# Kernel optimization log

Measured on AMD Instinct MI355X. Metric: run time of the kernel, lower is better.

## Reference

```python
import jax, jax.numpy as jnp
import numpy as np

HEADS = (4, 2, 1)
OUTS = (32, 16, 2)
NEG_SLOPE = 0.2


def gat_conv(x, src, dst, W, att_s, att_d, b, heads, out_dim, n_nodes, concat):
    # x: [N, Fin] -> h: [N, H, Fout]
    h = (x @ W).reshape(n_nodes, heads, out_dim)
    # per-node attention terms, gathered to edges: [E, H]
    a_src = jnp.sum(h * att_s, axis=-1)
    a_dst = jnp.sum(h * att_d, axis=-1)
    logits = jax.nn.leaky_relu(a_src[src] + a_dst[dst], NEG_SLOPE)
    # segment softmax over incoming edges of each destination node
    lmax = jax.ops.segment_max(logits, dst, num_segments=n_nodes)[dst]
    e = jnp.exp(logits - lmax)
    denom = jax.ops.segment_sum(e, dst, num_segments=n_nodes)[dst]
    alpha = e / denom  # [E, H]
    # weighted message aggregation
    msg = h[src] * alpha[:, :, None]  # [E, H, Fout]
    agg = jax.ops.segment_sum(msg, dst, num_segments=n_nodes)  # [N, H, Fout]
    if concat:
        agg = agg.reshape(n_nodes, heads * out_dim)
    else:
        agg = agg.mean(axis=1)
    return agg + b


def _glorot(key, shape):
    fan = shape[0] + shape[-1] if len(shape) == 2 else shape[-1] * 2
    s = jnp.sqrt(6.0 / fan)
    return jax.random.uniform(key, shape, jnp.float32, -s, s)


def setup_inputs() -> dict:
    key = jax.random.key(0)
    N, E, FIN = 100000, 1600000, 128
    ks = jax.random.split(key, 16)
    x = jax.random.normal(ks[0], (N, FIN), jnp.float32)
    edge_index = jax.random.randint(ks[1], (2, E), 0, N, jnp.int64)
    ins = (FIN, HEADS[0] * OUTS[0], HEADS[1] * OUTS[1])
    d = {"x": x, "edge_index": edge_index}
    for i in range(3):
        H, O = HEADS[i], OUTS[i]
        d[f"W{i+1}"] = _glorot(ks[2 + 4 * i], (ins[i], H * O))
        d[f"att_s{i+1}"] = _glorot(ks[3 + 4 * i], (H, O))
        d[f"att_d{i+1}"] = _glorot(ks[4 + 4 * i], (H, O))
        bdim = H * O if i < 2 else O
        d[f"b{i+1}"] = jnp.zeros((bdim,), jnp.float32)
    return d


def reference(x, edge_index, W1, att_s1, att_d1, b1, W2, att_s2, att_d2, b2, W3, att_s3, att_d3, b3):
    N = x.shape[0]
    loops = jnp.arange(N, dtype=edge_index.dtype)
    src = jnp.concatenate([edge_index[0], loops])
    dst = jnp.concatenate([edge_index[1], loops])
    h = gat_conv(x, src, dst, W1, att_s1, att_d1, b1, HEADS[0], OUTS[0], N, True)
    h = jax.nn.elu(h)
    h = gat_conv(h, src, dst, W2, att_s2, att_d2, b2, HEADS[1], OUTS[1], N, True)
    h = jax.nn.elu(h)
    h = gat_conv(h, src, dst, W3, att_s3, att_d3, b3, HEADS[2], OUTS[2], N, False)
    return jax.nn.log_softmax(h, axis=1)
```

## Files before the change

kernel.cpp:

```cpp
#include <hip/hip_runtime.h>
#include <math.h>

static __device__ __forceinline__ float lrelu(float x){ return fmaxf(x, 0.2f*x); }
static __device__ __forceinline__ float eluf(float x){ return x > 0.f ? x : __expf(x)-1.f; }
static __device__ __forceinline__ float wred_sum(float v){
  v += __shfl_xor(v, 32); v += __shfl_xor(v, 16); v += __shfl_xor(v, 8);
  v += __shfl_xor(v, 4);  v += __shfl_xor(v, 2);  v += __shfl_xor(v, 1);
  return v;
}
static __device__ __forceinline__ unsigned short f2bf(float f){
  unsigned int u = __float_as_uint(f);
  unsigned int r = (u + 0x7FFFu + ((u>>16)&1u)) >> 16;
  return (unsigned short)r;
}
static __device__ __forceinline__ float bflo(unsigned int u){ return __uint_as_float(u<<16); }
static __device__ __forceinline__ float bfhi(unsigned int u){ return __uint_as_float(u & 0xFFFF0000u); }

typedef __attribute__((ext_vector_type(8))) short short8;
typedef __attribute__((ext_vector_type(4))) float f32x4;

#define DETECT_IS64(ei_, s_is64_) \
  if (threadIdx.x < 64){ \
    int w_ = ((const int*)(ei_))[2*threadIdx.x + 1]; \
    unsigned long long b_ = __ballot(w_ != 0); \
    if (threadIdx.x == 0) s_is64_ = (b_ == 0ull); \
  } \
  __syncthreads();

__global__ __launch_bounds__(256) void k_bhist(const void* __restrict__ ei,
    int* __restrict__ gbcnt, int E, int NB){
  extern __shared__ int lcnt[];
  __shared__ int s_is64;
  for (int i=threadIdx.x; i<NB; i+=256) lcnt[i]=0;
  DETECT_IS64(ei, s_is64)
  int stride = gridDim.x*256;
  if (s_is64){
    const long long* p = (const long long*)ei;
    for (int e = blockIdx.x*256 + threadIdx.x; e < E; e += stride)
      atomicAdd(&lcnt[((int)p[(size_t)E+e])>>7], 1);
  } else {
    const int* p = (const int*)ei;
    for (int e = blockIdx.x*256 + threadIdx.x; e < E; e += stride)
      atomicAdd(&lcnt[p[(size_t)E+e]>>7], 1);
  }
  __syncthreads();
  for (int i=threadIdx.x; i<NB; i+=256){
    int c = lcnt[i];
    if (c) atomicAdd(&gbcnt[i], c);
  }
}

__global__ __launch_bounds__(256) void k_bscan(const int* __restrict__ gbcnt,
    int* __restrict__ gbbase, int* __restrict__ gcursor, int NB){
  __shared__ int sh[256];
  __shared__ int carry;
  int t = threadIdx.x;
  if (t==0) carry = 0;
  __syncthreads();
  for (int base=0; base<NB; base+=256){
    int idx = base+t;
    int v = (idx<NB)? gbcnt[idx] : 0;
    sh[t]=v; __syncthreads();
    for (int off=1; off<256; off<<=1){
      int add = (t>=off)? sh[t-off] : 0;
      __syncthreads();
      sh[t]+=add;
      __syncthreads();
    }
    int excl = sh[t]-v+carry;
    if (idx<NB){ gbbase[idx]=excl; gcursor[idx]=excl; }
    __syncthreads();
    if (t==0) carry += sh[255];
    __syncthreads();
  }
}

#define BS_ITEMS 16
__global__ __launch_bounds__(256) void k_scat_gemm1(
    const void* __restrict__ ei, int* __restrict__ gcursor,
    unsigned int* __restrict__ ebuf, int E, int NB, int GS,
    const float* __restrict__ x, const unsigned short* __restrict__ wf,
    const float* __restrict__ atts, const float* __restrict__ attd,
    unsigned short* __restrict__ hb, float* __restrict__ as_, float* __restrict__ ad_,
    int N){
  __shared__ __align__(16) unsigned char smem[50176];
  __shared__ int s_is64;
  int t = threadIdx.x;
  if ((int)blockIdx.x < GS){
    int* lcnt  = (int*)smem;
    int* lbase = lcnt + NB;
    for (int i=t; i<NB; i+=256) lcnt[i]=0;
    DETECT_IS64(ei, s_is64)
    bool is64 = s_is64 != 0;
    int base = blockIdx.x*(256*BS_ITEMS);
    unsigned int ent[BS_ITEMS]; int bk[BS_ITEMS];
    #pragma unroll
    for (int i=0;i<BS_ITEMS;i++){
      int e = base + i*256 + t;
      if (e < E){
        int s, d;
        if (is64){ const long long* p=(const long long*)ei; s=(int)p[e]; d=(int)p[(size_t)E+e]; }
        else     { const int* p=(const int*)ei;            s=p[e];      d=p[(size_t)E+e]; }
        int b = d>>7;
        bk[i] = b;
        ent[i] = (unsigned int)s | ((unsigned int)(d & 127) << 25);
        atomicAdd(&lcnt[b], 1);
      } else bk[i] = -1;
    }
    __syncthreads();
    for (int i=t; i<NB; i+=256){
      int c = lcnt[i];
      lbase[i] = c ? atomicAdd(&gcursor[i], c) : 0;
    }
    __syncthreads();
    for (int i=t; i<NB; i+=256) lcnt[i]=0;
    __syncthreads();
    #pragma unroll
    for (int i=0;i<BS_ITEMS;i++){
      if (bk[i] >= 0){
        int pos = lbase[bk[i]] + atomicAdd(&lcnt[bk[i]], 1);
        ebuf[pos] = ent[i];
      }
    }
  } else {
    unsigned short* xs  = (unsigned short*)smem;
    unsigned short* wsm = (unsigned short*)(smem + 64*136*2);
    int r0 = ((int)blockIdx.x - GS)*64;
    {
      const uint4* src = (const uint4*)wf;
      uint4* dst = (uint4*)wsm;
      #pragma unroll
      for (int i=0;i<8;i++) dst[t + i*256] = src[t + i*256];
    }
    {
      #pragma unroll
      for (int i=0;i<4;i++){
        int idx = t + i*256;
        int row = idx>>4, k8 = (idx&15)*8;
        int gr = r0 + row;
        float4 v0 = make_float4(0.f,0.f,0.f,0.f), v1 = v0;
        if (gr < N){
          v0 = *(const float4*)&x[(size_t)gr*128 + k8];
          v1 = *(const float4*)&x[(size_t)gr*128 + k8 + 4];
        }
        union { unsigned short us[8]; uint4 u; } pk;
        pk.us[0]=f2bf(v0.x); pk.us[1]=f2bf(v0.y); pk.us[2]=f2bf(v0.z); pk.us[3]=f2bf(v0.w);
        pk.us[4]=f2bf(v1.x); pk.us[5]=f2bf(v1.y); pk.us[6]=f2bf(v1.z); pk.us[7]=f2bf(v1.w);
        *(uint4*)&xs[row*136 + k8] = pk.u;
      }
    }
    __syncthreads();
    int w = t>>6, lane = t&63, lm = lane&15, q = lane>>4;
    int rt0 = (w&1)*2;
    int ct0 = (w>>1)*4;
    f32x4 acc[2][4];
    #pragma unroll
    for (int a=0;a<2;a++)
      #pragma unroll
      for (int c=0;c<4;c++) acc[a][c] = (f32x4){0.f,0.f,0.f,0.f};
    #pragma unroll
    for (int ks=0;ks<4;ks++){
      short8 a0 = *(const short8*)&xs[( rt0   *16 + lm)*136 + ks*32 + q*8];
      short8 a1 = *(const short8*)&xs[((rt0+1)*16 + lm)*136 + ks*32 + q*8];
      #pragma unroll
      for (int c=0;c<4;c++){
        short8 b = *(const short8*)&wsm[((ks*8 + ct0 + c)*64 + lane)*8];
        acc[0][c] = __builtin_amdgcn_mfma_f32_16x16x32_bf16(a0, b, acc[0][c], 0,0,0);
        acc[1][c] = __builtin_amdgcn_mfma_f32_16x16x32_bf16(a1, b, acc[1][c], 0,0,0);
      }
    }
    __syncthreads();
    #pragma unroll
    for (int rl=0;rl<2;rl++)
      #pragma unroll
      for (int c=0;c<4;c++)
        #pragma unroll
        for (int r=0;r<4;r++)
          xs[((rt0+rl)*16 + q*4 + r)*136 + (ct0+c)*16 + lm] = f2bf(acc[rl][c][r]);
    __syncthreads();
    {
      #pragma unroll
      for (int i=0;i<4;i++){
        int idx = t + i*256;
        int row = idx>>4, c8 = (idx&15)*8;
        int gr = r0 + row;
        if (gr < N)
          *(uint4*)&hb[(size_t)gr*128 + c8] = *(const uint4*)&xs[row*136 + c8];
      }
    }
    {
      int row = t>>2, h = t&3;
      int gr = r0 + row;
      if (gr < N){
        const unsigned short* hr = &xs[row*136 + h*32];
        const float* sa = atts + h*32;
        const float* da = attd + h*32;
        float ss = 0.f, dd = 0.f;
        #pragma unroll
        for (int o=0;o<32;o+=8){
          uint4 v = *(const uint4*)&hr[o];
          float hv[8] = { bflo(v.x),bfhi(v.x),bflo(v.y),bfhi(v.y),
                          bflo(v.z),bfhi(v.z),bflo(v.w),bfhi(v.w) };
          #pragma unroll
          for (int m=0;m<8;m++){ ss += hv[m]*sa[o+m]; dd += hv[m]*da[o+m]; }
        }
        as_[gr*4+h] = ss; ad_[gr*4+h] = dd;
      }
    }
  }
}

__global__ __launch_bounds__(256) void k_bcsr(const unsigned int* __restrict__ ebuf,
    const int* __restrict__ gbbase, const int* __restrict__ gbcnt,
    int* __restrict__ rp, int* __restrict__ csr, int N, int NB, int E){
  __shared__ int lcnt[128];
  __shared__ int lexc[128];
  __shared__ int lcur[128];
  __shared__ int sc[256];
  int b = blockIdx.x, t = threadIdx.x;
  int d0 = b<<7;
  int R = N - d0; if (R > 128) R = 128;
  if (t < 128){ lcnt[t]=0; lcur[t]=0; }
  __syncthreads();
  int base = gbbase[b], cnt = gbcnt[b];
  for (int i=t; i<cnt; i+=256){
    unsigned int e = ebuf[base+i];
    atomicAdd(&lcnt[e>>25], 1);
  }
  __syncthreads();
  int v = (t<128)? lcnt[t] : 0;
  sc[t]=v; __syncthreads();
  for (int off=1; off<128; off<<=1){
    int add = (t>=off)? sc[t-off] : 0;
    __syncthreads();
    sc[t]+=add;
    __syncthreads();
  }
  if (t<128) lexc[t] = sc[t]-v;
  __syncthreads();
  if (t < R) rp[d0+t] = base + lexc[t];
  if (b == NB-1 && t == 0) rp[N] = E;
  for (int i=t; i<cnt; i+=256){
    unsigned int e = ebuf[base+i];
    int dl = e>>25;
    int pos = base + lexc[dl] + atomicAdd(&lcur[dl], 1);
    csr[pos] = (int)(e & 0x1FFFFFFu);
  }
}

__global__ void k_wprep(const float* __restrict__ W1, const float* __restrict__ W2,
                        unsigned short* __restrict__ wf1, unsigned short* __restrict__ wf2){
  int e = blockIdx.x*256 + threadIdx.x;
  if (e < 2048){
    int lane = e&63, ct = (e>>6)&7, ks = e>>9;
    int q = lane>>4, n = lane&15;
    union { unsigned short us[8]; uint4 u; } pk;
    #pragma unroll
    for (int j=0;j<8;j++)
      pk.us[j] = f2bf(W1[(ks*32 + q*8 + j)*128 + ct*16 + n]);
    *(uint4*)&wf1[(size_t)e*8] = pk.u;
  } else if (e < 2048+512){
    int e2 = e - 2048;
    int lane = e2&63, ct = (e2>>6)&1, ks = e2>>7;
    int q = lane>>4, n = lane&15;
    union { unsigned short us[8]; uint4 u; } pk;
    #pragma unroll
    for (int j=0;j<8;j++)
      pk.us[j] = f2bf(W2[(ks*32 + q*8 + j)*32 + ct*16 + n]);
    *(uint4*)&wf2[(size_t)e2*8] = pk.u;
  }
}

__global__ __launch_bounds__(256) void k_mgemm2(const unsigned short* __restrict__ xb,
    const unsigned short* __restrict__ wf,
    const float* __restrict__ atts, const float* __restrict__ attd,
    unsigned short* __restrict__ hb2, float* __restrict__ as_, float* __restrict__ ad_,
    int N){
  __shared__ unsigned short xs[128*136];
  __shared__ unsigned short wsm[512*8];
  int t = threadIdx.x;
  int r0 = blockIdx.x*128;
  {
    #pragma unroll
    for (int i=0;i<2;i++)
      ((uint4*)wsm)[t + i*256] = ((const uint4*)wf)[t + i*256];
  }
  {
    #pragma unroll
    for (int i=0;i<8;i++){
      int idx = t + i*256;
      int row = idx>>4, c8 = (idx&15)*8;
      int gr = r0 + row;
      uint4 v = make_uint4(0u,0u,0u,0u);
      if (gr < N) v = *(const uint4*)&xb[(size_t)gr*128 + c8];
      *(uint4*)&xs[row*136 + c8] = v;
    }
  }
  __syncthreads();
  int w = t>>6, lane = t&63, lm = lane&15, q = lane>>4;
  int rt0 = 2*w;
  f32x4 acc[2][2];
  #pragma unroll
  for (int a=0;a<2;a++){ acc[a][0] = (f32x4){0.f,0.f,0.f,0.f}; acc[a][1] = acc[a][0]; }
  #pragma unroll
  for (int ks=0;ks<4;ks++){
    short8 a0 = *(const short8*)&xs[( rt0   *16 + lm)*136 + ks*32 + q*8];
    short8 a1 = *(const short8*)&xs[((rt0+1)*16 + lm)*136 + ks*32 + q*8];
    #pragma unroll
    for (int c=0;c<2;c++){
      short8 b = *(const short8*)&wsm[((ks*2 + c)*64 + lane)*8];
      acc[0][c] = __builtin_amdgcn_mfma_f32_16x16x32_bf16(a0, b, acc[0][c], 0,0,0);
      acc[1][c] = __builtin_amdgcn_mfma_f32_16x16x32_bf16(a1, b, acc[1][c], 0,0,0);
    }
  }
  __syncthreads();
  #pragma unroll
  for (int rl=0;rl<2;rl++)
    #pragma unroll
    for (int c=0;c<2;c++)
      #pragma unroll
      for (int r=0;r<4;r++)
        xs[((rt0+rl)*16 + q*4 + r)*136 + c*16 + lm] = f2bf(acc[rl][c][r]);
  __syncthreads();
  {
    #pragma unroll
    for (int i=0;i<2;i++){
      int idx = t + i*256;
      int row = idx>>2, c8 = (idx&3)*8;
      int gr = r0 + row;
      if (gr < N)
        *(uint4*)&hb2[(size_t)gr*32 + c8] = *(const uint4*)&xs[row*136 + c8];
    }
  }
  {
    int row = t>>1, h = t&1;
    int gr = r0 + row;
    if (gr < N){
      const unsigned short* hr = &xs[row*136 + h*16];
      const float* sa = atts + h*16;
      const float* da = attd + h*16;
      float ss = 0.f, dd = 0.f;
      #pragma unroll
      for (int o=0;o<16;o+=8){
        uint4 v = *(const uint4*)&hr[o];
        float hv[8] = { bflo(v.x),bfhi(v.x),bflo(v.y),bfhi(v.y),
                        bflo(v.z),bfhi(v.z),bflo(v.w),bfhi(v.w) };
        #pragma unroll
        for (int m=0;m<8;m++){ ss += hv[m]*sa[o+m]; dd += hv[m]*da[o+m]; }
      }
      as_[gr*2+h] = ss; ad_[gr*2+h] = dd;
    }
  }
}

__global__ __launch_bounds__(256) void k_agg1(const int* __restrict__ rp, const int* __restrict__ csr,
    const float* __restrict__ as_, const float* __restrict__ ad_,
    const uint4* __restrict__ hb4, const float* __restrict__ bias,
    unsigned short* __restrict__ outb, int N){
  int n = blockIdx.x*4 + (threadIdx.x>>6);
  if (n >= N) return;
  int lane = threadIdx.x & 63;
  int eslot = lane>>2, ehead = lane&3;
  int grp = lane>>4, li = lane&15, ghead = li>>2;
  int start = rp[n], end = rp[n+1];
  float adh_e = ad_[n*4+ehead];
  float w_self_e = __expf(fminf(lrelu(as_[n*4+ehead] + adh_e), 80.f));
  float l = (eslot == 0) ? w_self_e : 0.f;
  float a[8];
  #pragma unroll
  for (int k=0;k<8;k++) a[k]=0.f;
  {
    float w = __shfl(w_self_e, ghead);
    if (grp == 0){
      uint4 v = hb4[(size_t)n*16 + li];
      a[0]+=w*bflo(v.x); a[1]+=w*bfhi(v.x); a[2]+=w*bflo(v.y); a[3]+=w*bfhi(v.y);
      a[4]+=w*bflo(v.z); a[5]+=w*bfhi(v.z); a[6]+=w*bflo(v.w); a[7]+=w*bfhi(v.w);
    }
  }
  for (int i0 = start; i0 < end; i0 += 32){
    int ei0 = i0 + eslot, ei1 = i0 + 16 + eslot;
    int s0 = -1, s1 = -1; float w0 = 0.f, w1 = 0.f;
    if (ei0 < end){
      s0 = csr[ei0];
      w0 = __expf(fminf(lrelu(as_[s0*4+ehead] + adh_e), 80.f));
      l += w0;
    }
    if (ei1 < end){
      s1 = csr[ei1];
      w1 = __expf(fminf(lrelu(as_[s1*4+ehead] + adh_e), 80.f));
      l += w1;
    }
    #pragma unroll
    for (int r=0;r<4;r++){
      int srclane = ((r*4+grp)<<2) | ghead;
      int   s2 = __shfl(s0, srclane);
      float w2 = __shfl(w0, srclane);
      int   s3 = __shfl(s1, srclane);
      float w3 = __shfl(w1, srclane);
      if (s2 >= 0){
        uint4 v = hb4[(size_t)s2*16 + li];
        a[0]+=w2*bflo(v.x); a[1]+=w2*bfhi(v.x); a[2]+=w2*bflo(v.y); a[3]+=w2*bfhi(v.y);
        a[4]+=w2*bflo(v.z); a[5]+=w2*bfhi(v.z); a[6]+=w2*bflo(v.w); a[7]+=w2*bfhi(v.w);
      }
      if (s3 >= 0){
        uint4 v = hb4[(size_t)s3*16 + li];
        a[0]+=w3*bflo(v.x); a[1]+=w3*bfhi(v.x); a[2]+=w3*bflo(v.y); a[3]+=w3*bfhi(v.y);
        a[4]+=w3*bflo(v.z); a[5]+=w3*bfhi(v.z); a[6]+=w3*bflo(v.w); a[7]+=w3*bfhi(v.w);
      }
    }
  }
  l += __shfl_xor(l,4); l += __shfl_xor(l,8); l += __shfl_xor(l,16); l += __shfl_xor(l,32);
  #pragma unroll
  for (int msk=16; msk<64; msk<<=1){
    #pragma unroll
    for (int k=0;k<8;k++) a[k] += __shfl_xor(a[k], msk);
  }
  float denom = __shfl(l, ghead);
  if (grp == 0){
    float invh = 1.f/denom;
    float4 b0 = *(const float4*)&bias[li*8];
    float4 b1 = *(const float4*)&bias[li*8+4];
    union { unsigned short us[8]; uint4 v; } pk;
    pk.us[0]=f2bf(eluf(a[0]*invh+b0.x)); pk.us[1]=f2bf(eluf(a[1]*invh+b0.y));
    pk.us[2]=f2bf(eluf(a[2]*invh+b0.z)); pk.us[3]=f2bf(eluf(a[3]*invh+b0.w));
    pk.us[4]=f2bf(eluf(a[4]*invh+b1.x)); pk.us[5]=f2bf(eluf(a[5]*invh+b1.y));
    pk.us[6]=f2bf(eluf(a[6]*invh+b1.z)); pk.us[7]=f2bf(eluf(a[7]*invh+b1.w));
    *(uint4*)&outb[(size_t)n*128 + li*8] = pk.v;
  }
}

__global__ __launch_bounds__(256) void k_agg2(const int* __restrict__ rp, const int* __restrict__ csr,
    const float* __restrict__ as_, const float* __restrict__ ad_,
    const uint4* __restrict__ hb4, const float* __restrict__ bias,
    const float* __restrict__ W3, const float* __restrict__ atts3,
    const float* __restrict__ attd3,
    float* __restrict__ h3, float* __restrict__ as3_, float* __restrict__ ad3_,
    int N){
  int n = blockIdx.x*4 + (threadIdx.x>>6);
  if (n >= N) return;
  int lane = threadIdx.x & 63;
  int eslot = lane>>1, ehead = lane&1;
  int grp = lane>>2, li = lane&3, ghead = li>>1;
  int start = rp[n], end = rp[n+1];
  float adh_e = ad_[n*2+ehead];
  float w_self_e = __expf(fminf(lrelu(as_[n*2+ehead] + adh_e), 80.f));
  float l = (eslot == 0) ? w_self_e : 0.f;
  float a[8];
  #pragma unroll
  for (int k=0;k<8;k++) a[k]=0.f;
  {
    float w = __shfl(w_self_e, ghead);
    if (grp == 0){
      uint4 v = hb4[(size_t)n*4 + li];
      a[0]+=w*bflo(v.x); a[1]+=w*bfhi(v.x); a[2]+=w*bflo(v.y); a[3]+=w*bfhi(v.y);
      a[4]+=w*bflo(v.z); a[5]+=w*bfhi(v.z); a[6]+=w*bflo(v.w); a[7]+=w*bfhi(v.w);
    }
  }
  for (int i0 = start; i0 < end; i0 += 64){
    int ei0 = i0 + eslot, ei1 = i0 + 32 + eslot;
    int s0 = -1, s1 = -1; float w0 = 0.f, w1 = 0.f;
    if (ei0 < end){
      s0 = csr[ei0];
      w0 = __expf(fminf(lrelu(as_[s0*2+ehead] + adh_e), 80.f));
      l += w0;
    }
    if (ei1 < end){
      s1 = csr[ei1];
      w1 = __expf(fminf(lrelu(as_[s1*2+ehead] + adh_e), 80.f));
      l += w1;
    }
    #pragma unroll
    for (int r=0;r<2;r++){
      int srclane = ((r*16+grp)<<1) | ghead;
      int   s2 = __shfl(s0, srclane);
      float w2 = __shfl(w0, srclane);
      int   s3 = __shfl(s1, srclane);
      float w3 = __shfl(w1, srclane);
      if (s2 >= 0){
        uint4 v = hb4[(size_t)s2*4 + li];
        a[0]+=w2*bflo(v.x); a[1]+=w2*bfhi(v.x); a[2]+=w2*bflo(v.y); a[3]+=w2*bfhi(v.y);
        a[4]+=w2*bflo(v.z); a[5]+=w2*bfhi(v.z); a[6]+=w2*bflo(v.w); a[7]+=w2*bfhi(v.w);
      }
      if (s3 >= 0){
        uint4 v = hb4[(size_t)s3*4 + li];
        a[0]+=w3*bflo(v.x); a[1]+=w3*bfhi(v.x); a[2]+=w3*bflo(v.y); a[3]+=w3*bfhi(v.y);
        a[4]+=w3*bflo(v.z); a[5]+=w3*bfhi(v.z); a[6]+=w3*bflo(v.w); a[7]+=w3*bfhi(v.w);
      }
    }
  }
  l += __shfl_xor(l,2); l += __shfl_xor(l,4); l += __shfl_xor(l,8);
  l += __shfl_xor(l,16); l += __shfl_xor(l,32);
  #pragma unroll
  for (int msk=4; msk<64; msk<<=1){
    #pragma unroll
    for (int k=0;k<8;k++) a[k] += __shfl_xor(a[k], msk);
  }
  float denom = __shfl(l, ghead);
  float invh = 1.f/denom;
  float r0_ = eluf(a[0]*invh + bias[li*8+0]);
  float r1_ = eluf(a[1]*invh + bias[li*8+1]);
  float r2_ = eluf(a[2]*invh + bias[li*8+2]);
  float r3_ = eluf(a[3]*invh + bias[li*8+3]);
  float r4_ = eluf(a[4]*invh + bias[li*8+4]);
  float r5_ = eluf(a[5]*invh + bias[li*8+5]);
  float r6_ = eluf(a[6]*invh + bias[li*8+6]);
  float r7_ = eluf(a[7]*invh + bias[li*8+7]);
  const float* wr = &W3[li*16];
  float p0 = r0_*wr[0] + r1_*wr[2] + r2_*wr[4]  + r3_*wr[6]
           + r4_*wr[8] + r5_*wr[10]+ r6_*wr[12] + r7_*wr[14];
  float p1 = r0_*wr[1] + r1_*wr[3] + r2_*wr[5]  + r3_*wr[7]
           + r4_*wr[9] + r5_*wr[11]+ r6_*wr[13] + r7_*wr[15];
  p0 += __shfl_xor(p0,1); p0 += __shfl_xor(p0,2);
  p1 += __shfl_xor(p1,1); p1 += __shfl_xor(p1,2);
  if (lane == 0){
    h3[2*n] = p0; h3[2*n+1] = p1;
    as3_[n] = p0*atts3[0] + p1*atts3[1];
    ad3_[n] = p0*attd3[0] + p1*attd3[1];
  }
}

__global__ __launch_bounds__(256) void k_agg3(const int* __restrict__ rp, const int* __restrict__ csr,
    const float* __restrict__ as_, const float* __restrict__ ad_,
    const float* __restrict__ h, const float* __restrict__ bias,
    float* __restrict__ out, int N){
  int n = blockIdx.x*4 + (threadIdx.x>>6);
  if (n >= N) return;
  int lane = threadIdx.x & 63;
  int start = rp[n], end = rp[n+1];
  float adh = ad_[n];
  float sl = lrelu(as_[n] + adh);
  const float2* h2 = (const float2*)h;
  float l = 0.f;
  float2 acc = make_float2(0.f, 0.f);
  for (int i=start+lane; i<end; i+=64){
    int s = csr[i];
    float w = __expf(fminf(lrelu(as_[s] + adh), 80.f));
    l += w;
    float2 v = h2[s];
    acc.x += w*v.x; acc.y += w*v.y;
  }
  if (lane == 0){
    float w = __expf(fminf(sl, 80.f));
    l += w;
    float2 v = h2[n];
    acc.x += w*v.x; acc.y += w*v.y;
  }
  l = wred_sum(l);
  acc.x = wred_sum(acc.x); acc.y = wred_sum(acc.y);
  if (lane == 0){
    float inv = 1.f/l;
    float g0 = acc.x*inv + bias[0];
    float g1 = acc.y*inv + bias[1];
    float mm = fmaxf(g0, g1);
    float lse = mm + logf(__expf(g0-mm) + __expf(g1-mm));
    *(float2*)&out[2*n] = make_float2(g0-lse, g1-lse);
  }
}

extern "C" void kernel_launch(void* const* d_in, const int* in_sizes, int n_in,
                              void* d_out, int out_size, void* d_ws, size_t ws_size,
                              hipStream_t stream) {
  const float* x   = (const float*)d_in[0];
  const void*  ei  = d_in[1];
  const float* W1  = (const float*)d_in[2];
  const float* as1 = (const float*)d_in[3];
  const float* ad1 = (const float*)d_in[4];
  const float* b1  = (const float*)d_in[5];
  const float* W2  = (const float*)d_in[6];
  const float* as2 = (const float*)d_in[7];
  const float* ad2 = (const float*)d_in[8];
  const float* b2  = (const float*)d_in[9];
  const float* W3  = (const float*)d_in[10];
  const float* as3 = (const float*)d_in[11];
  const float* ad3 = (const float*)d_in[12];
  const float* b3  = (const float*)d_in[13];

  int N = in_sizes[0] / 128;
  int E = in_sizes[1] / 2;
  int NB = (N + 127) >> 7;

  char* w = (char*)d_ws;
  size_t off = 0;
  auto alloc = [&](size_t bytes)->void*{
    void* p = w + off; off += (bytes + 255) & ~(size_t)255; return p;
  };
  int*   gbcnt   = (int*)alloc((size_t)NB*4);
  int*   gbbase  = (int*)alloc((size_t)NB*4);
  int*   gcursor = (int*)alloc((size_t)NB*4);
  int*   rp      = (int*)alloc((size_t)(N+1)*4);
  unsigned int* ebuf = (unsigned int*)alloc((size_t)E*4);
  int*   csr     = (int*)alloc((size_t)E*4);
  float* as_buf  = (float*)alloc((size_t)N*4*4);
  float* ad_buf  = (float*)alloc((size_t)N*4*4);
  float* as3_buf = (float*)alloc((size_t)N*4);
  float* ad3_buf = (float*)alloc((size_t)N*4);
  unsigned short* wf1 = (unsigned short*)alloc(2048*8*2);
  unsigned short* wf2 = (unsigned short*)alloc(512*8*2);
  unsigned short* hb  = (unsigned short*)alloc((size_t)N*128*2);
  unsigned short* xb  = (unsigned short*)alloc((size_t)N*128*2);
  unsigned short* hb2 = (unsigned short*)alloc((size_t)N*32*2);
  float* h3      = (float*)alloc((size_t)N*2*4);
  if (off > ws_size) return;

  hipMemsetAsync(gbcnt, 0, (size_t)NB*4, stream);
  k_wprep<<<10, 256, 0, stream>>>(W1, W2, wf1, wf2);
  k_bhist<<<256, 256, NB*4, stream>>>(ei, gbcnt, E, NB);
  k_bscan<<<1, 256, 0, stream>>>(gbcnt, gbbase, gcursor, NB);

  int GS = (E + 256*BS_ITEMS - 1) / (256*BS_ITEMS);
  int G1 = (N + 63)/64;
  k_scat_gemm1<<<GS + G1, 256, 0, stream>>>(ei, gcursor, ebuf, E, NB, GS,
                                            x, wf1, as1, ad1, hb, as_buf, ad_buf, N);
  k_bcsr<<<NB, 256, 0, stream>>>(ebuf, gbbase, gbcnt, rp, csr, N, NB, E);

  k_agg1<<<(N + 3)/4, 256, 0, stream>>>(rp, csr, as_buf, ad_buf, (const uint4*)hb, b1, xb, N);

  k_mgemm2<<<(N + 127)/128, 256, 0, stream>>>(xb, wf2, as2, ad2, hb2, as_buf, ad_buf, N);
  k_agg2<<<(N + 3)/4, 256, 0, stream>>>(rp, csr, as_buf, ad_buf, (const uint4*)hb2, b2,
                                        W3, as3, ad3, h3, as3_buf, ad3_buf, N);

  k_agg3<<<(N + 3)/4, 256, 0, stream>>>(rp, csr, as3_buf, ad3_buf, h3, b3, (float*)d_out, N);
}
```

Baseline: 356.5 us.

## Fuse layer-2 GEMM into layer-1 aggregation and pack layer-3 node data

Each wave in the layer-1 aggregation now applies bias and ELU and multiplies its 128-wide row by W2 in fp32 through shuffle reductions. It writes hb2 and the layer-2 attention scalars directly, which removes the bf16 xb intermediate round trip, the k_mgemm2 MFMA kernel and one launch. Layer-3 per-node values (h, a_src, a_dst) are packed into a single float4 so each gathered edge in k_agg3 needs one 16-byte load instead of separate loads. The trade-off is extra per-node ALU and shuffle work plus W2 reads from global/cache inside the latency-bound aggregation, replacing tensor-core matrix ops.

```diff
diff --git a/kernel.cpp b/kernel.cpp
--- a/kernel.cpp
+++ b/kernel.cpp
@@ -248,8 +248,7 @@
   }
 }
 
-__global__ void k_wprep(const float* __restrict__ W1, const float* __restrict__ W2,
-                        unsigned short* __restrict__ wf1, unsigned short* __restrict__ wf2){
+__global__ void k_wprep(const float* __restrict__ W1, unsigned short* __restrict__ wf1){
   int e = blockIdx.x*256 + threadIdx.x;
   if (e < 2048){
     int lane = e&63, ct = (e>>6)&7, ks = e>>9;
@@ -259,104 +258,16 @@
     for (int j=0;j<8;j++)
       pk.us[j] = f2bf(W1[(ks*32 + q*8 + j)*128 + ct*16 + n]);
     *(uint4*)&wf1[(size_t)e*8] = pk.u;
-  } else if (e < 2048+512){
-    int e2 = e - 2048;
-    int lane = e2&63, ct = (e2>>6)&1, ks = e2>>7;
-    int q = lane>>4, n = lane&15;
-    union { unsigned short us[8]; uint4 u; } pk;
-    #pragma unroll
-    for (int j=0;j<8;j++)
-      pk.us[j] = f2bf(W2[(ks*32 + q*8 + j)*32 + ct*16 + n]);
-    *(uint4*)&wf2[(size_t)e2*8] = pk.u;
-  }
-}
-
-__global__ __launch_bounds__(256) void k_mgemm2(const unsigned short* __restrict__ xb,
-    const unsigned short* __restrict__ wf,
-    const float* __restrict__ atts, const float* __restrict__ attd,
-    unsigned short* __restrict__ hb2, float* __restrict__ as_, float* __restrict__ ad_,
-    int N){
-  __shared__ unsigned short xs[128*136];
-  __shared__ unsigned short wsm[512*8];
-  int t = threadIdx.x;
-  int r0 = blockIdx.x*128;
-  {
-    #pragma unroll
-    for (int i=0;i<2;i++)
-      ((uint4*)wsm)[t + i*256] = ((const uint4*)wf)[t + i*256];
-  }
-  {
-    #pragma unroll
-    for (int i=0;i<8;i++){
-      int idx = t + i*256;
-      int row = idx>>4, c8 = (idx&15)*8;
-      int gr = r0 + row;
-      uint4 v = make_uint4(0u,0u,0u,0u);
-      if (gr < N) v = *(const uint4*)&xb[(size_t)gr*128 + c8];
-      *(uint4*)&xs[row*136 + c8] = v;
-    }
-  }
-  __syncthreads();
-  int w = t>>6, lane = t&63, lm = lane&15, q = lane>>4;
-  int rt0 = 2*w;
-  f32x4 acc[2][2];
-  #pragma unroll
-  for (int a=0;a<2;a++){ acc[a][0] = (f32x4){0.f,0.f,0.f,0.f}; acc[a][1] = acc[a][0]; }
-  #pragma unroll
-  for (int ks=0;ks<4;ks++){
-    short8 a0 = *(const short8*)&xs[( rt0   *16 + lm)*136 + ks*32 + q*8];
-    short8 a1 = *(const short8*)&xs[((rt0+1)*16 + lm)*136 + ks*32 + q*8];
-    #pragma unroll
-    for (int c=0;c<2;c++){
-      short8 b = *(const short8*)&wsm[((ks*2 + c)*64 + lane)*8];
-      acc[0][c] = __builtin_amdgcn_mfma_f32_16x16x32_bf16(a0, b, acc[0][c], 0,0,0);
-      acc[1][c] = __builtin_amdgcn_mfma_f32_16x16x32_bf16(a1, b, acc[1][c], 0,0,0);
-    }
-  }
-  __syncthreads();
-  #pragma unroll
-  for (int rl=0;rl<2;rl++)
-    #pragma unroll
-    for (int c=0;c<2;c++)
-      #pragma unroll
-      for (int r=0;r<4;r++)
-        xs[((rt0+rl)*16 + q*4 + r)*136 + c*16 + lm] = f2bf(acc[rl][c][r]);
-  __syncthreads();
-  {
-    #pragma unroll
-    for (int i=0;i<2;i++){
-      int idx = t + i*256;
-      int row = idx>>2, c8 = (idx&3)*8;
-      int gr = r0 + row;
-      if (gr < N)
-        *(uint4*)&hb2[(size_t)gr*32 + c8] = *(const uint4*)&xs[row*136 + c8];
-    }
-  }
-  {
-    int row = t>>1, h = t&1;
-    int gr = r0 + row;
-    if (gr < N){
-      const unsigned short* hr = &xs[row*136 + h*16];
-      const float* sa = atts + h*16;
-      const float* da = attd + h*16;
-      float ss = 0.f, dd = 0.f;
-      #pragma unroll
-      for (int o=0;o<16;o+=8){
-        uint4 v = *(const uint4*)&hr[o];
-        float hv[8] = { bflo(v.x),bfhi(v.x),bflo(v.y),bfhi(v.y),
-                        bflo(v.z),bfhi(v.z),bflo(v.w),bfhi(v.w) };
-        #pragma unroll
-        for (int m=0;m<8;m++){ ss += hv[m]*sa[o+m]; dd += hv[m]*da[o+m]; }
-      }
-      as_[gr*2+h] = ss; ad_[gr*2+h] = dd;
-    }
   }
 }
 
 __global__ __launch_bounds__(256) void k_agg1(const int* __restrict__ rp, const int* __restrict__ csr,
     const float* __restrict__ as_, const float* __restrict__ ad_,
     const uint4* __restrict__ hb4, const float* __restrict__ bias,
-    unsigned short* __restrict__ outb, int N){
+    const float* __restrict__ W2, const float* __restrict__ atts2,
+    const float* __restrict__ attd2,
+    unsigned short* __restrict__ hb2, float* __restrict__ as2_, float* __restrict__ ad2_,
+    int N){
   int n = blockIdx.x*4 + (threadIdx.x>>6);
   if (n >= N) return;
   int lane = threadIdx.x & 63;
@@ -416,16 +327,44 @@
     for (int k=0;k<8;k++) a[k] += __shfl_xor(a[k], msk);
   }
   float denom = __shfl(l, ghead);
-  if (grp == 0){
-    float invh = 1.f/denom;
-    float4 b0 = *(const float4*)&bias[li*8];
-    float4 b1 = *(const float4*)&bias[li*8+4];
-    union { unsigned short us[8]; uint4 v; } pk;
-    pk.us[0]=f2bf(eluf(a[0]*invh+b0.x)); pk.us[1]=f2bf(eluf(a[1]*invh+b0.y));
-    pk.us[2]=f2bf(eluf(a[2]*invh+b0.z)); pk.us[3]=f2bf(eluf(a[3]*invh+b0.w));
-    pk.us[4]=f2bf(eluf(a[4]*invh+b1.x)); pk.us[5]=f2bf(eluf(a[5]*invh+b1.y));
-    pk.us[6]=f2bf(eluf(a[6]*invh+b1.z)); pk.us[7]=f2bf(eluf(a[7]*invh+b1.w));
-    *(uint4*)&outb[(size_t)n*128 + li*8] = pk.v;
+  float invh = 1.f/denom;
+  float r[8];
+  #pragma unroll
+  for (int k=0;k<8;k++) r[k] = eluf(a[k]*invh + bias[li*8+k]);
+  float p[8];
+  #pragma unroll
+  for (int c=0;c<8;c++) p[c]=0.f;
+  #pragma unroll
+  for (int j=0;j<8;j++){
+    const float4* wrow = (const float4*)&W2[(li*8+j)*32 + grp*8];
+    float4 w0 = wrow[0], w1 = wrow[1];
+    float rv = r[j];
+    p[0]+=rv*w0.x; p[1]+=rv*w0.y; p[2]+=rv*w0.z; p[3]+=rv*w0.w;
+    p[4]+=rv*w1.x; p[5]+=rv*w1.y; p[6]+=rv*w1.z; p[7]+=rv*w1.w;
+  }
+  #pragma unroll
+  for (int msk=1; msk<16; msk<<=1){
+    #pragma unroll
+    for (int c=0;c<8;c++) p[c] += __shfl_xor(p[c], msk);
+  }
+  if (li == 0){
+    union { unsigned short us[8]; uint4 v; } pk2;
+    #pragma unroll
+    for (int c=0;c<8;c++) pk2.us[c] = f2bf(p[c]);
+    *(uint4*)&hb2[(size_t)n*32 + grp*8] = pk2.v;
+  }
+  {
+    int h2h = grp>>1, ob = (grp&1)*8;
+    const float* sa = atts2 + h2h*16 + ob;
+    const float* da = attd2 + h2h*16 + ob;
+    float ss=0.f, dd=0.f;
+    #pragma unroll
+    for (int c=0;c<8;c++){ ss += p[c]*sa[c]; dd += p[c]*da[c]; }
+    ss += __shfl_xor(ss, 16); dd += __shfl_xor(dd, 16);
+    if (li == 0 && (grp&1)==0){
+      as2_[n*2 + h2h] = ss;
+      ad2_[n*2 + h2h] = dd;
+    }
   }
 }
 
@@ -434,8 +373,7 @@
     const uint4* __restrict__ hb4, const float* __restrict__ bias,
     const float* __restrict__ W3, const float* __restrict__ atts3,
     const float* __restrict__ attd3,
-    float* __restrict__ h3, float* __restrict__ as3_, float* __restrict__ ad3_,
-    int N){
+    float4* __restrict__ pk4, int N){
   int n = blockIdx.x*4 + (threadIdx.x>>6);
   if (n >= N) return;
   int lane = threadIdx.x & 63;
@@ -513,37 +451,37 @@
   p0 += __shfl_xor(p0,1); p0 += __shfl_xor(p0,2);
   p1 += __shfl_xor(p1,1); p1 += __shfl_xor(p1,2);
   if (lane == 0){
-    h3[2*n] = p0; h3[2*n+1] = p1;
-    as3_[n] = p0*atts3[0] + p1*atts3[1];
-    ad3_[n] = p0*attd3[0] + p1*attd3[1];
+    float4 pk;
+    pk.x = p0; pk.y = p1;
+    pk.z = p0*atts3[0] + p1*atts3[1];
+    pk.w = p0*attd3[0] + p1*attd3[1];
+    pk4[n] = pk;
   }
 }
 
 __global__ __launch_bounds__(256) void k_agg3(const int* __restrict__ rp, const int* __restrict__ csr,
-    const float* __restrict__ as_, const float* __restrict__ ad_,
-    const float* __restrict__ h, const float* __restrict__ bias,
+    const float4* __restrict__ pk4, const float* __restrict__ bias,
     float* __restrict__ out, int N){
   int n = blockIdx.x*4 + (threadIdx.x>>6);
   if (n >= N) return;
   int lane = threadIdx.x & 63;
   int start = rp[n], end = rp[n+1];
-  float adh = ad_[n];
-  float sl = lrelu(as_[n] + adh);
-  const float2* h2 = (const float2*)h;
+  float4 self = pk4[n];
+  float adh = self.w;
+  float sl = lrelu(self.z + adh);
   float l = 0.f;
   float2 acc = make_float2(0.f, 0.f);
   for (int i=start+lane; i<end; i+=64){
     int s = csr[i];
-    float w = __expf(fminf(lrelu(as_[s] + adh), 80.f));
+    float4 ps = pk4[s];
+    float w = __expf(fminf(lrelu(ps.z + adh), 80.f));
     l += w;
-    float2 v = h2[s];
-    acc.x += w*v.x; acc.y += w*v.y;
+    acc.x += w*ps.x; acc.y += w*ps.y;
   }
   if (lane == 0){
     float w = __expf(fminf(sl, 80.f));
     l += w;
-    float2 v = h2[n];
-    acc.x += w*v.x; acc.y += w*v.y;
+    acc.x += w*self.x; acc.y += w*self.y;
   }
   l = wred_sum(l);
   acc.x = wred_sum(acc.x); acc.y = wred_sum(acc.y);
@@ -592,18 +530,16 @@
   int*   csr     = (int*)alloc((size_t)E*4);
   float* as_buf  = (float*)alloc((size_t)N*4*4);
   float* ad_buf  = (float*)alloc((size_t)N*4*4);
-  float* as3_buf = (float*)alloc((size_t)N*4);
-  float* ad3_buf = (float*)alloc((size_t)N*4);
+  float* as2_buf = (float*)alloc((size_t)N*2*4);
+  float* ad2_buf = (float*)alloc((size_t)N*2*4);
   unsigned short* wf1 = (unsigned short*)alloc(2048*8*2);
-  unsigned short* wf2 = (unsigned short*)alloc(512*8*2);
   unsigned short* hb  = (unsigned short*)alloc((size_t)N*128*2);
-  unsigned short* xb  = (unsigned short*)alloc((size_t)N*128*2);
   unsigned short* hb2 = (unsigned short*)alloc((size_t)N*32*2);
-  float* h3      = (float*)alloc((size_t)N*2*4);
+  float4* pk4    = (float4*)alloc((size_t)N*16);
   if (off > ws_size) return;
 
   hipMemsetAsync(gbcnt, 0, (size_t)NB*4, stream);
-  k_wprep<<<10, 256, 0, stream>>>(W1, W2, wf1, wf2);
+  k_wprep<<<8, 256, 0, stream>>>(W1, wf1);
   k_bhist<<<256, 256, NB*4, stream>>>(ei, gbcnt, E, NB);
   k_bscan<<<1, 256, 0, stream>>>(gbcnt, gbbase, gcursor, NB);
 
@@ -613,11 +549,11 @@
                                             x, wf1, as1, ad1, hb, as_buf, ad_buf, N);
   k_bcsr<<<NB, 256, 0, stream>>>(ebuf, gbbase, gbcnt, rp, csr, N, NB, E);
 
-  k_agg1<<<(N + 3)/4, 256, 0, stream>>>(rp, csr, as_buf, ad_buf, (const uint4*)hb, b1, xb, N);
-
-  k_mgemm2<<<(N + 127)/128, 256, 0, stream>>>(xb, wf2, as2, ad2, hb2, as_buf, ad_buf, N);
-  k_agg2<<<(N + 3)/4, 256, 0, stream>>>(rp, csr, as_buf, ad_buf, (const uint4*)hb2, b2,
-                                        W3, as3, ad3, h3, as3_buf, ad3_buf, N);
-
-  k_agg3<<<(N + 3)/4, 256, 0, stream>>>(rp, csr, as3_buf, ad3_buf, h3, b3, (float*)d_out, N);
-}
+  k_agg1<<<(N + 3)/4, 256, 0, stream>>>(rp, csr, as_buf, ad_buf, (const uint4*)hb, b1,
+                                        W2, as2, ad2, hb2, as2_buf, ad2_buf, N);
+
+  k_agg2<<<(N + 3)/4, 256, 0, stream>>>(rp, csr, as2_buf, ad2_buf, (const uint4*)hb2, b2,
+                                        W3, as3, ad3, pk4, N);
+
+  k_agg3<<<(N + 3)/4, 256, 0, stream>>>(rp, csr, pk4, b3, (float*)d_out, N);
+}
```

New measurement: 484.8 us. 1.36x slower.
